# Kernel optimization log

Measured on AMD Instinct MI355X. Metric: run time of the kernel, lower is better.

Reference implementation:

```python
import jax, jax.numpy as jnp
import numpy as np

# Problem sizes (batched graph of G molecules)
N = 100_000   # total nodes
E = 400_000   # total directed edges
G = 2_500     # number of molecule graphs
K = 3         # len(idx_wo_smiles) -> zero rows inserted
NODE_F = 74   # graph_feats_shape[0]
EDGE_F = 12   # graph_feats_shape[1]
HID = 128     # hidden_feats = dim // 2
DIM = 256     # dim


def setup_inputs() -> dict:
    key = jax.random.key(0)
    ks = jax.random.split(key, 20)
    init = lambda k, shape, fan: (jax.random.normal(k, shape, jnp.float32) / np.sqrt(fan)).astype(jnp.float32)

    node_feats = jax.random.normal(ks[0], (N, NODE_F), jnp.float32)
    edge_feats = jax.random.normal(ks[1], (E, EDGE_F), jnp.float32)  # passed but unused by GCN
    src = jax.random.randint(ks[2], (E,), 0, N)
    dst = jax.random.randint(ks[3], (E,), 0, N)
    # sorted graph ids, every graph non-empty (~40 atoms each)
    graph_ids = (jnp.arange(N) * G) // N
    idx_wo_smiles = jnp.arange(K)

    return {
        'node_feats': node_feats,
        'edge_feats': edge_feats,
        'W1': init(ks[4], (NODE_F, HID), NODE_F), 'b1': jnp.zeros((HID,), jnp.float32),
        'Wr1': init(ks[5], (NODE_F, HID), NODE_F), 'br1': jnp.zeros((HID,), jnp.float32),
        'W2': init(ks[6], (HID, HID), HID), 'b2': jnp.zeros((HID,), jnp.float32),
        'Wr2': init(ks[7], (HID, HID), HID), 'br2': jnp.zeros((HID,), jnp.float32),
        'w_atom': init(ks[8], (HID, 1), HID), 'b_atom': jnp.zeros((1,), jnp.float32),
        'Wp1': init(ks[9], (2 * HID, HID), 2 * HID), 'bp1': jnp.zeros((HID,), jnp.float32),
        'Wp2': init(ks[10], (HID, DIM), HID), 'bp2': jnp.zeros((DIM,), jnp.float32),
        'src': src, 'dst': dst, 'graph_ids': graph_ids, 'idx_wo_smiles': idx_wo_smiles,
    }


def reference(node_feats, edge_feats, W1, b1, Wr1, br1, W2, b2, Wr2, br2,
              w_atom, b_atom, Wp1, bp1, Wp2, bp2, src, dst, graph_ids, idx_wo_smiles):
    n = node_feats.shape[0]
    ones_e = jnp.ones(src.shape[0], jnp.float32)
    out_deg = jax.ops.segment_sum(ones_e, src, num_segments=n)
    in_deg = jax.ops.segment_sum(ones_e, dst, num_segments=n)
    norm_s = jax.lax.rsqrt(jnp.maximum(out_deg, 1.0))  # [N]
    norm_d = jax.lax.rsqrt(jnp.maximum(in_deg, 1.0))   # [N]

    def gcn_layer(h, W, b, Wr, br):
        # GraphConv(norm='both'): D^-1/2 A D^-1/2 h W + b, with relu activation
        m = h[src] * norm_s[src][:, None]                       # [E, F] gather
        agg = jax.ops.segment_sum(m, dst, num_segments=n)       # [N, F] scatter-add
        gc = jax.nn.relu((agg * norm_d[:, None]) @ W + b)
        res = jax.nn.relu(h @ Wr + br)                          # residual connection
        return gc + res

    h = gcn_layer(node_feats, W1, b1, Wr1, br1)   # [N, HID]
    h = gcn_layer(h, W2, b2, Wr2, br2)            # [N, HID]

    # WeightedSumAndMax readout per molecule
    aw = jax.nn.sigmoid(h @ w_atom + b_atom)                          # [N, 1]
    hsum = jax.ops.segment_sum(h * aw, graph_ids, num_segments=G)     # [G, HID]
    hmax = jax.ops.segment_max(h, graph_ids, num_segments=G)          # [G, HID]
    gfeat = jnp.concatenate([hsum, hmax], axis=1)                     # [G, 2*HID]

    latent = jax.nn.relu(gfeat @ Wp1 + bp1) @ Wp2 + bp2               # [G, DIM]

    # Insert zero rows at idx_wo_smiles (sorted ascending -> final positions)
    total = G + idx_wo_smiles.shape[0]
    zero_mask = jnp.zeros((total,), bool).at[idx_wo_smiles].set(True)
    keep = jnp.nonzero(~zero_mask, size=G)[0]
    out = jnp.zeros((total, latent.shape[1]), latent.dtype).at[keep].set(latent)
    return out
```

## Files before the change

### kernel.cpp

```cpp
#include <hip/hip_runtime.h>
#include <hip/hip_bf16.h>
#include <stdint.h>

#define NODE_F 74
#define HID 128
#define DIM 256

typedef __hip_bfloat16 bf16;
typedef unsigned int u32;
typedef unsigned short u16;

typedef short s16x8 __attribute__((ext_vector_type(8)));
typedef __bf16 bf16x8 __attribute__((ext_vector_type(8)));
typedef float f32x4 __attribute__((ext_vector_type(4)));

__device__ __forceinline__ float rdl(float v, int l){
  return __int_as_float(__builtin_amdgcn_readlane(__float_as_int(v), l));
}
__device__ __forceinline__ float2 bfpair(u32 u){
  float2 r;
  r.x = __uint_as_float(u << 16);
  r.y = __uint_as_float(u & 0xffff0000u);
  return r;
}
__device__ __forceinline__ u32 packbf(float a, float b){
  u32 lo = (u32)__bfloat16_as_ushort(__float2bfloat16(a));
  u32 hi = (u32)__bfloat16_as_ushort(__float2bfloat16(b));
  return lo | (hi << 16);
}
__device__ __forceinline__ u16 bfbits(float a){
  return __bfloat16_as_ushort(__float2bfloat16(a));
}

__global__ void k_deg_prep(const int* __restrict__ src, const int* __restrict__ dst_,
                           float* __restrict__ outdeg_f, int* __restrict__ indeg, int E_,
                           const float* __restrict__ W1, const float* __restrict__ Wr1,
                           const float* __restrict__ W2, const float* __restrict__ Wr2,
                           u16* __restrict__ Bp1, u16* __restrict__ Bp2){
  int e = blockIdx.x*256 + threadIdx.x;
  if (e < E_){
    atomicAdd(&outdeg_f[src[e]], 1.0f);
    atomicAdd(&indeg[dst_[e]], 1);
  }
  int idx = e;
  if (idx < 57344){
    const float* W; u16* dstp; int S, Ktrue, loc;
    if      (idx < 12288){ W = W1;  dstp = Bp1;          S = 3; Ktrue = NODE_F; loc = idx; }
    else if (idx < 24576){ W = Wr1; dstp = Bp1 + 12288;  S = 3; Ktrue = NODE_F; loc = idx - 12288; }
    else if (idx < 40960){ W = W2;  dstp = Bp2;          S = 4; Ktrue = HID;    loc = idx - 24576; }
    else                 { W = Wr2; dstp = Bp2 + 16384;  S = 4; Ktrue = HID;    loc = idx - 40960; }
    const int el  = loc & 7;
    const int l   = (loc >> 3) & 63;
    const int rem = loc >> 9;
    const int s   = rem % S;
    const int t   = rem / S;
    const int k   = s*32 + (l >> 4)*8 + el;
    const int c   = t*16 + (l & 15);
    const float v = (k < Ktrue) ? W[(size_t)k*HID + c] : 0.f;
    dstp[loc] = bfbits(v);
  }
}

__global__ __launch_bounds__(256) void k_scan_a(const int* __restrict__ indeg,
                                                float* __restrict__ norm_s,
                                                float* __restrict__ norm_d,
                                                int* __restrict__ bsum, int n){
  __shared__ int red[256];
  const int base = blockIdx.x*1024 + threadIdx.x*4;
  int s = 0;
  #pragma unroll
  for (int i = 0; i < 4; ++i){
    const int idx = base + i;
    if (idx < n){
      const int d = indeg[idx];
      s += d;
      norm_d[idx] = rsqrtf(fmaxf((float)d, 1.0f));
      norm_s[idx] = rsqrtf(fmaxf(norm_s[idx], 1.0f));
    }
  }
  red[threadIdx.x] = s;
  __syncthreads();
  #pragma unroll
  for (int off = 128; off; off >>= 1){
    if (threadIdx.x < off) red[threadIdx.x] += red[threadIdx.x + off];
    __syncthreads();
  }
  if (threadIdx.x == 0) bsum[blockIdx.x] = red[0];
}

__global__ __launch_bounds__(1024) void k_scan_b(int* __restrict__ bsum, int nb){
  __shared__ int part[1024];
  __shared__ int carry;
  if (threadIdx.x == 0) carry = 0;
  __syncthreads();
  for (int c0 = 0; c0 < nb; c0 += 1024){
    const int tid = threadIdx.x, idx = c0 + tid;
    part[tid] = (idx < nb) ? bsum[idx] : 0;
    __syncthreads();
    for (int off = 1; off < 1024; off <<= 1){
      const int t = (tid >= off) ? part[tid-off] : 0;
      __syncthreads();
      part[tid] += t;
      __syncthreads();
    }
    if (idx < nb) bsum[idx] = carry + ((tid == 0) ? 0 : part[tid-1]);
    __syncthreads();
    if (tid == 0) carry += part[1023];
    __syncthreads();
  }
}

__global__ __launch_bounds__(256) void k_scan_c(int* __restrict__ indeg,
                                                const int* __restrict__ bsum,
                                                int* __restrict__ row_ptr, int n){
  __shared__ int part[256];
  const int base = blockIdx.x*1024 + threadIdx.x*4;
  int v[4]; int s = 0;
  #pragma unroll
  for (int i = 0; i < 4; ++i){
    const int idx = base + i;
    v[i] = (idx < n) ? indeg[idx] : 0;
    s += v[i];
  }
  part[threadIdx.x] = s;
  __syncthreads();
  for (int off = 1; off < 256; off <<= 1){
    const int t = (threadIdx.x >= off) ? part[threadIdx.x-off] : 0;
    __syncthreads();
    part[threadIdx.x] += t;
    __syncthreads();
  }
  int run = bsum[blockIdx.x] + ((threadIdx.x == 0) ? 0 : part[threadIdx.x-1]);
  #pragma unroll
  for (int i = 0; i < 4; ++i){
    const int idx = base + i;
    if (idx < n){
      row_ptr[idx] = run;
      run += v[i];
      indeg[idx] = 0;
    }
    if (idx == n-1) row_ptr[n] = run;
  }
}

__global__ void k_fill_conv(const int* __restrict__ src, const int* __restrict__ dst,
                            const int* __restrict__ row_ptr, int* __restrict__ cursor,
                            int* __restrict__ col, int E_,
                            const float* __restrict__ x0,
                            const float* __restrict__ norm_s,
                            u32* __restrict__ x0bf, int n, int do_conv){
  int e = blockIdx.x*256 + threadIdx.x;
  if (e < E_){
    int d = dst[e];
    int pos = row_ptr[d] + atomicAdd(&cursor[d], 1);
    col[pos] = src[e];
  }
  if (do_conv){
    const int tot = n*48;
    if (e < tot){
      const int r = e/48, l = e - r*48;
      const int f0 = 2*l, f1 = 2*l + 1;
      const float ns = norm_s[r];
      const float u0 = (f0 < NODE_F) ? ns*x0[(size_t)r*NODE_F + f0] : 0.f;
      const float u1 = (f1 < NODE_F) ? ns*x0[(size_t)r*NODE_F + f1] : 0.f;
      x0bf[e] = packbf(u0, u1);
    }
  }
}

__global__ __launch_bounds__(256, 8) void k_gather1b(
    const u32* __restrict__ x0bf, const int* __restrict__ row_ptr,
    const int* __restrict__ col, const float* __restrict__ norm_d,
    u32* __restrict__ ag1, int n){
  const int lane = threadIdx.x & 63;
  const int wv   = (blockIdx.x*256 + threadIdx.x) >> 6;
  const int r0   = wv*2;
  if (r0 >= n) return;
  int p[2], e[2];
  p[0] = row_ptr[r0]; e[0] = row_ptr[r0+1];
  const bool ok1 = (r0+1) < n;
  p[1] = ok1 ? e[0] : 0;
  e[1] = ok1 ? row_ptr[r0+2] : 0;
  const bool act = (lane < 48);
  const u32* xb = x0bf + lane;
  float a0[2] = {0.f,0.f}, a1[2] = {0.f,0.f};
  while ((p[0] < e[0]) | (p[1] < e[1])){
    int c[2], s[2][4];
    #pragma unroll
    for (int i = 0; i < 2; ++i){
      int d = e[i] - p[i];
      c[i] = (d > 4) ? 4 : ((d < 0) ? 0 : d);
      if (c[i] > 0){
        #pragma unroll
        for (int j = 0; j < 4; ++j)
          s[i][j] = col[p[i] + ((j < c[i]) ? j : (c[i]-1))];
      }
    }
    u32 v[2][4];
    #pragma unroll
    for (int i = 0; i < 2; ++i){
      #pragma unroll
      for (int j = 0; j < 4; ++j) v[i][j] = 0u;
      if (c[i] > 0 && act){
        #pragma unroll
        for (int j = 0; j < 4; ++j){
          const u32 t = xb[(size_t)s[i][j]*48];
          v[i][j] = (j < c[i]) ? t : 0u;
        }
      }
    }
    #pragma unroll
    for (int i = 0; i < 2; ++i){
      const float2 f0 = bfpair(v[i][0]), f1 = bfpair(v[i][1]);
      const float2 f2 = bfpair(v[i][2]), f3 = bfpair(v[i][3]);
      a0[i] += (f0.x + f1.x) + (f2.x + f3.x);
      a1[i] += (f0.y + f1.y) + (f2.y + f3.y);
      p[i] += c[i];
    }
  }
  if (lane < 48){
    #pragma unroll
    for (int i = 0; i < 2; ++i){
      const int row = r0 + i;
      if (row < n){
        const float nd = norm_d[row];
        ag1[(size_t)row*48 + lane] = packbf(a0[i]*nd, a1[i]*nd);
      }
    }
  }
}

__global__ __launch_bounds__(256, 8) void k_gather2b(
    const u32* __restrict__ h1u, const int* __restrict__ row_ptr,
    const int* __restrict__ col, const float* __restrict__ norm_s,
    const float* __restrict__ norm_d, u32* __restrict__ ag2, int n){
  const int lane = threadIdx.x & 63;
  const int wv   = (blockIdx.x*256 + threadIdx.x) >> 6;
  const int r0   = wv*2;
  if (r0 >= n) return;
  int p[2], e[2];
  p[0] = row_ptr[r0]; e[0] = row_ptr[r0+1];
  const bool ok1 = (r0+1) < n;
  p[1] = ok1 ? e[0] : 0;
  e[1] = ok1 ? row_ptr[r0+2] : 0;
  const u32* hb = h1u + lane;
  float a0[2] = {0.f,0.f}, a1[2] = {0.f,0.f};
  while ((p[0] < e[0]) | (p[1] < e[1])){
    int c[2], s[2][4];
    #pragma unroll
    for (int i = 0; i < 2; ++i){
      int d = e[i] - p[i];
      c[i] = (d > 4) ? 4 : ((d < 0) ? 0 : d);
      if (c[i] > 0){
        #pragma unroll
        for (int j = 0; j < 4; ++j)
          s[i][j] = col[p[i] + ((j < c[i]) ? j : (c[i]-1))];
      }
    }
    float nw[2][4];
    u32 v[2][4];
    #pragma unroll
    for (int i = 0; i < 2; ++i){
      #pragma unroll
      for (int j = 0; j < 4; ++j){ nw[i][j] = 0.f; v[i][j] = 0u; }
      if (c[i] > 0){
        #pragma unroll
        for (int j = 0; j < 4; ++j) nw[i][j] = (j < c[i]) ? norm_s[s[i][j]] : 0.f;
        #pragma unroll
        for (int j = 0; j < 4; ++j) v[i][j] = hb[(size_t)s[i][j]*64];
      }
    }
    #pragma unroll
    for (int i = 0; i < 2; ++i){
      const float2 f0 = bfpair(v[i][0]), f1 = bfpair(v[i][1]);
      const float2 f2 = bfpair(v[i][2]), f3 = bfpair(v[i][3]);
      a0[i] = fmaf(f0.x, nw[i][0], fmaf(f1.x, nw[i][1],
              fmaf(f2.x, nw[i][2], fmaf(f3.x, nw[i][3], a0[i]))));
      a1[i] = fmaf(f0.y, nw[i][0], fmaf(f1.y, nw[i][1],
              fmaf(f2.y, nw[i][2], fmaf(f3.y, nw[i][3], a1[i]))));
      p[i] += c[i];
    }
  }
  #pragma unroll
  for (int i = 0; i < 2; ++i){
    const int row = r0 + i;
    if (row < n){
      const float nd = norm_d[row];
      ag2[(size_t)row*64 + lane] = packbf(a0[i]*nd, a1[i]*nd);
    }
  }
}

__global__ __launch_bounds__(256) void k_gather1f(
    const float* __restrict__ x0, const int* __restrict__ row_ptr,
    const int* __restrict__ col, const float* __restrict__ norm_s,
    const float* __restrict__ norm_d, u32* __restrict__ ag1, int n){
  const int lane = threadIdx.x & 63;
  const int row  = blockIdx.x*4 + (threadIdx.x >> 6);
  if (row >= n) return;
  const int p0 = row_ptr[row], p1 = row_ptr[row+1];
  const bool act = (lane < 37);
  const float* xb = x0 + 2*lane;
  float a0 = 0.f, a1 = 0.f;
  int p = p0;
  #pragma unroll 1
  for (; p + 3 < p1; p += 4){
    const int s0 = col[p], s1 = col[p+1], s2 = col[p+2], s3 = col[p+3];
    const float n0 = norm_s[s0], n1 = norm_s[s1], n2 = norm_s[s2], n3 = norm_s[s3];
    float2 v0{0.f,0.f}, v1{0.f,0.f}, v2{0.f,0.f}, v3{0.f,0.f};
    if (act){
      v0 = *(const float2*)&xb[(size_t)s0*NODE_F];
      v1 = *(const float2*)&xb[(size_t)s1*NODE_F];
      v2 = *(const float2*)&xb[(size_t)s2*NODE_F];
      v3 = *(const float2*)&xb[(size_t)s3*NODE_F];
    }
    a0 = fmaf(v0.x,n0, fmaf(v1.x,n1, fmaf(v2.x,n2, fmaf(v3.x,n3, a0))));
    a1 = fmaf(v0.y,n0, fmaf(v1.y,n1, fmaf(v2.y,n2, fmaf(v3.y,n3, a1))));
  }
  const int rem = p1 - p;
  if (rem > 0){
    const int s0 = col[p];
    int s1 = s0, s2 = s0;
    float n1 = 0.f, n2 = 0.f;
    const float n0 = norm_s[s0];
    if (rem > 1){ s1 = col[p+1]; n1 = norm_s[s1]; }
    if (rem > 2){ s2 = col[p+2]; n2 = norm_s[s2]; }
    float2 v0{0.f,0.f}, v1{0.f,0.f}, v2{0.f,0.f};
    if (act){
      v0 = *(const float2*)&xb[(size_t)s0*NODE_F];
      v1 = *(const float2*)&xb[(size_t)s1*NODE_F];
      v2 = *(const float2*)&xb[(size_t)s2*NODE_F];
    }
    a0 = fmaf(v0.x,n0, fmaf(v1.x,n1, fmaf(v2.x,n2, a0)));
    a1 = fmaf(v0.y,n0, fmaf(v1.y,n1, fmaf(v2.y,n2, a1)));
  }
  if (lane < 48){
    const float nd = norm_d[row];
    ag1[(size_t)row*48 + lane] = packbf(a0*nd, a1*nd);
  }
}

__global__ __launch_bounds__(256) void k_gather2f(
    const u32* __restrict__ h1u, const int* __restrict__ row_ptr,
    const int* __restrict__ col, const float* __restrict__ norm_s,
    const float* __restrict__ norm_d, u32* __restrict__ ag2, int n){
  const int lane = threadIdx.x & 63;
  const int row  = blockIdx.x*4 + (threadIdx.x >> 6);
  if (row >= n) return;
  const int p0 = row_ptr[row], p1 = row_ptr[row+1];
  const u32* hb = h1u + lane;
  float a0 = 0.f, a1 = 0.f;
  int p = p0;
  #pragma unroll 1
  for (; p + 3 < p1; p += 4){
    const int s0 = col[p], s1 = col[p+1], s2 = col[p+2], s3 = col[p+3];
    const float n0 = norm_s[s0], n1 = norm_s[s1], n2 = norm_s[s2], n3 = norm_s[s3];
    const u32 u0 = hb[(size_t)s0*64];
    const u32 u1 = hb[(size_t)s1*64];
    const u32 u2 = hb[(size_t)s2*64];
    const u32 u3 = hb[(size_t)s3*64];
    const float2 f0 = bfpair(u0), f1 = bfpair(u1), f2 = bfpair(u2), f3 = bfpair(u3);
    a0 = fmaf(f0.x,n0, fmaf(f1.x,n1, fmaf(f2.x,n2, fmaf(f3.x,n3, a0))));
    a1 = fmaf(f0.y,n0, fmaf(f1.y,n1, fmaf(f2.y,n2, fmaf(f3.y,n3, a1))));
  }
  const int rem = p1 - p;
  if (rem > 0){
    const int s0 = col[p];
    int s1 = s0, s2 = s0;
    float n1 = 0.f, n2 = 0.f;
    const float n0 = norm_s[s0];
    if (rem > 1){ s1 = col[p+1]; n1 = norm_s[s1]; }
    if (rem > 2){ s2 = col[p+2]; n2 = norm_s[s2]; }
    const u32 u0 = hb[(size_t)s0*64];
    const u32 u1 = hb[(size_t)s1*64];
    const u32 u2 = hb[(size_t)s2*64];
    const float2 f0 = bfpair(u0), f1 = bfpair(u1), f2 = bfpair(u2);
    a0 = fmaf(f0.x,n0, fmaf(f1.x,n1, fmaf(f2.x,n2, a0)));
    a1 = fmaf(f0.y,n0, fmaf(f1.y,n1, fmaf(f2.y,n2, a1)));
  }
  const float nd = norm_d[row];
  ag2[(size_t)row*64 + lane] = packbf(a0*nd, a1*nd);
}

__global__ __launch_bounds__(256) void k_ggemm1(
    const u16* __restrict__ ag1, const float* __restrict__ x0,
    const u16* __restrict__ Bp, const float* __restrict__ bg_,
    const float* __restrict__ br_, u16* __restrict__ h1, int n){
  const int lane = threadIdx.x & 63;
  const int wid  = threadIdx.x >> 6;
  const int jg = lane & 15, kg = lane >> 4;
  const int r0 = blockIdx.x*64 + wid*16;
  const int row = r0 + jg;
  const bool rok = row < n;
  const int kb = kg*8;
  const int rA = rok ? row : (n-1);

  bf16x8 ag[3], ar[3];
  #pragma unroll
  for (int s = 0; s < 3; ++s)
    ag[s] = __builtin_bit_cast(bf16x8, *(const s16x8*)&ag1[(size_t)rA*96 + s*32 + kb]);
  {
    const float* px = x0 + (size_t)rA*NODE_F;
    #pragma unroll
    for (int s = 0; s < 2; ++s)
      #pragma unroll
      for (int e = 0; e < 8; e += 2){
        const float2 w = *(const float2*)&px[s*32 + kb + e];
        ar[s][e]   = (__bf16)w.x;
        ar[s][e+1] = (__bf16)w.y;
      }
    #pragma unroll
    for (int e = 0; e < 8; ++e) ar[2][e] = (__bf16)0.f;
    if (kg == 0){
      #pragma unroll
      for (int e = 0; e < 8; e += 2){
        const float2 w = *(const float2*)&px[64 + e];
        ar[2][e]   = (__bf16)w.x;
        ar[2][e+1] = (__bf16)w.y;
      }
    } else if (kg == 1){
      const float2 w = *(const float2*)&px[72];
      ar[2][0] = (__bf16)w.x;
      ar[2][1] = (__bf16)w.y;
    }
  }

  f32x4 accg[8], accr[8];
  #pragma unroll
  for (int t = 0; t < 8; ++t){
    accg[t] = f32x4{0.f,0.f,0.f,0.f};
    accr[t] = f32x4{0.f,0.f,0.f,0.f};
  }
  constexpr int FR1 = 8*3*512;
  #pragma unroll
  for (int s = 0; s < 3; ++s){
    #pragma unroll
    for (int t = 0; t < 8; ++t){
      const bf16x8 bg = __builtin_bit_cast(bf16x8,
          *(const s16x8*)&Bp[((t*3 + s)*64 + lane)*8]);
      const bf16x8 br = __builtin_bit_cast(bf16x8,
          *(const s16x8*)&Bp[FR1 + ((t*3 + s)*64 + lane)*8]);
      accg[t] = __builtin_amdgcn_mfma_f32_16x16x32_bf16(ag[s], bg, accg[t], 0,0,0);
      accr[t] = __builtin_amdgcn_mfma_f32_16x16x32_bf16(ar[s], br, accr[t], 0,0,0);
    }
  }

  const int rowb = r0 + 4*kg;
  #pragma unroll
  for (int t = 0; t < 8; ++t){
    const int colc = t*16 + jg;
    const float bgv = bg_[colc], brv = br_[colc];
    #pragma unroll
    for (int r = 0; r < 4; ++r){
      const int row2 = rowb + r;
      if (row2 < n){
        const float o = fmaxf(accg[t][r] + bgv, 0.f) + fmaxf(accr[t][r] + brv, 0.f);
        h1[(size_t)row2*HID + colc] = bfbits(o);
      }
    }
  }
}

__global__ __launch_bounds__(256) void k_ggemm2(
    const u16* __restrict__ ag2, const u16* __restrict__ h1,
    const u16* __restrict__ Bp, const float* __restrict__ bg_,
    const float* __restrict__ br_,
    const float* __restrict__ w_atom, const float* __restrict__ b_atom,
    const int* __restrict__ gid,
    float* __restrict__ hsum, u32* __restrict__ hmax, int n){
  const int lane = threadIdx.x & 63;
  const int wid  = threadIdx.x >> 6;
  const int jg = lane & 15, kg = lane >> 4;
  const int r0 = blockIdx.x*64 + wid*16;
  const int row = r0 + jg;
  const bool rok = row < n;
  const int kb = kg*8;
  const int rA = rok ? row : (n-1);

  f32x4 accg[8], accr[8];
  #pragma unroll
  for (int t = 0; t < 8; ++t){
    accg[t] = f32x4{0.f,0.f,0.f,0.f};
    accr[t] = f32x4{0.f,0.f,0.f,0.f};
  }
  constexpr int FR2 = 8*4*512;
  #pragma unroll
  for (int s = 0; s < 4; ++s){
    const bf16x8 agf = __builtin_bit_cast(bf16x8,
        *(const s16x8*)&ag2[(size_t)rA*HID + s*32 + kb]);
    const bf16x8 arf = __builtin_bit_cast(bf16x8,
        *(const s16x8*)&h1[(size_t)rA*HID + s*32 + kb]);
    #pragma unroll
    for (int t = 0; t < 8; ++t){
      const bf16x8 bg = __builtin_bit_cast(bf16x8,
          *(const s16x8*)&Bp[((t*4 + s)*64 + lane)*8]);
      const bf16x8 br = __builtin_bit_cast(bf16x8,
          *(const s16x8*)&Bp[FR2 + ((t*4 + s)*64 + lane)*8]);
      accg[t] = __builtin_amdgcn_mfma_f32_16x16x32_bf16(agf, bg, accg[t], 0,0,0);
      accr[t] = __builtin_amdgcn_mfma_f32_16x16x32_bf16(arf, br, accr[t], 0,0,0);
    }
  }

  float o[8][4];
  #pragma unroll
  for (int t = 0; t < 8; ++t){
    const int colc = t*16 + jg;
    const float bgv = bg_[colc], brv = br_[colc];
    #pragma unroll
    for (int r = 0; r < 4; ++r)
      o[t][r] = fmaxf(accg[t][r] + bgv, 0.f) + fmaxf(accr[t][r] + brv, 0.f);
  }
  if (r0 < n){
    float wa[8];
    #pragma unroll
    for (int t = 0; t < 8; ++t) wa[t] = w_atom[t*16 + jg];
    const float ba = b_atom[0];
    const int rowb = r0 + 4*kg;
    float awv[4]; int gidr[4];
    #pragma unroll
    for (int r = 0; r < 4; ++r){
      const int row2 = rowb + r;
      float dot = 0.f;
      #pragma unroll
      for (int t = 0; t < 8; ++t) dot = fmaf(o[t][r], wa[t], dot);
      dot += __shfl_xor(dot, 1);
      dot += __shfl_xor(dot, 2);
      dot += __shfl_xor(dot, 4);
      dot += __shfl_xor(dot, 8);
      awv[r]  = 1.0f/(1.0f + __expf(-(dot + ba)));
      gidr[r] = (row2 < n) ? gid[row2] : -1;
    }
    const int rhi    = (r0 + 15 < n) ? (r0 + 15) : (n - 1);
    const int gfirst = gid[r0];
    const int glast  = gid[rhi];
    for (int g = gfirst; g <= glast; ++g){
      #pragma unroll
      for (int t = 0; t < 8; ++t){
        float sv = 0.f, mv = 0.f;
        #pragma unroll
        for (int r = 0; r < 4; ++r){
          const bool in = (gidr[r] == g);
          sv += in ? o[t][r]*awv[r] : 0.f;
          mv  = in ? fmaxf(mv, o[t][r]) : mv;
        }
        sv += __shfl_xor(sv, 16);
        sv += __shfl_xor(sv, 32);
        mv  = fmaxf(mv, __shfl_xor(mv, 16));
        mv  = fmaxf(mv, __shfl_xor(mv, 32));
        if (lane < 16){
          atomicAdd(&hsum[(size_t)g*HID + t*16 + jg], sv);
          atomicMax(&hmax[(size_t)g*HID + t*16 + jg], __float_as_uint(mv));
        }
      }
    }
  }
}

__global__ __launch_bounds__(256) void k_mlp(
    const float* __restrict__ hsum, const float* __restrict__ hmaxf,
    const float* __restrict__ Wp1, const float* __restrict__ bp1,
    const float* __restrict__ Wp2, const float* __restrict__ bp2,
    const int* __restrict__ idxw, int K_,
    float* __restrict__ out, int G_){
  const int lane = threadIdx.x & 63;
  const int row = blockIdx.x*4 + (threadIdx.x >> 6);
  if (blockIdx.x == 0){
    for (int j = 0; j < K_; ++j){
      const int zr = idxw[j];
      for (int i = threadIdx.x; i < DIM; i += 256)
        out[(size_t)zr*DIM + i] = 0.f;
    }
  }
  if (row >= G_) return;
  const int c = lane*2;
  float ra0 = hsum [(size_t)row*HID + lane];
  float ra1 = hsum [(size_t)row*HID + 64 + lane];
  float ra2 = hmaxf[(size_t)row*HID + lane];
  float ra3 = hmaxf[(size_t)row*HID + 64 + lane];
  float a0 = 0.f, a1 = 0.f;
  #pragma unroll 4
  for (int k = 0; k < 64; ++k){
    const float v0 = rdl(ra0,k), v1 = rdl(ra1,k), v2 = rdl(ra2,k), v3 = rdl(ra3,k);
    const float2 w0 = *(const float2*)&Wp1[(size_t)(k      )*HID + c];
    const float2 w1 = *(const float2*)&Wp1[(size_t)(k +  64)*HID + c];
    const float2 w2 = *(const float2*)&Wp1[(size_t)(k + 128)*HID + c];
    const float2 w3 = *(const float2*)&Wp1[(size_t)(k + 192)*HID + c];
    a0 = fmaf(v0,w0.x, fmaf(v1,w1.x, fmaf(v2,w2.x, fmaf(v3,w3.x, a0))));
    a1 = fmaf(v0,w0.y, fmaf(v1,w1.y, fmaf(v2,w2.y, fmaf(v3,w3.y, a1))));
  }
  const float h0  = fmaxf(a0 + bp1[c],   0.f);
  const float h1v = fmaxf(a1 + bp1[c+1], 0.f);
  const int c4 = lane*4;
  float acc0=0.f, acc1=0.f, acc2=0.f, acc3=0.f;
  #pragma unroll 4
  for (int j = 0; j < 64; ++j){
    const float he = rdl(h0, j);
    const float ho = rdl(h1v, j);
    const float4 we = *(const float4*)&Wp2[(size_t)(2*j  )*DIM + c4];
    const float4 wo = *(const float4*)&Wp2[(size_t)(2*j+1)*DIM + c4];
    acc0 = fmaf(he,we.x, fmaf(ho,wo.x, acc0));
    acc1 = fmaf(he,we.y, fmaf(ho,wo.y, acc1));
    acc2 = fmaf(he,we.z, fmaf(ho,wo.z, acc2));
    acc3 = fmaf(he,we.w, fmaf(ho,wo.w, acc3));
  }
  int orow = row;
  for (int j = 0; j < K_; ++j){ if (idxw[j] <= orow) orow++; }
  float* po = out + (size_t)orow*DIM + c4;
  po[0] = acc0 + bp2[c4];
  po[1] = acc1 + bp2[c4+1];
  po[2] = acc2 + bp2[c4+2];
  po[3] = acc3 + bp2[c4+3];
}

extern "C" void kernel_launch(void* const* d_in, const int* in_sizes, int n_in,
                              void* d_out, int out_size, void* d_ws, size_t ws_size,
                              hipStream_t stream){
  (void)n_in;
  const float* x0     = (const float*)d_in[0];
  const float* W1     = (const float*)d_in[2];
  const float* b1     = (const float*)d_in[3];
  const float* Wr1    = (const float*)d_in[4];
  const float* br1    = (const float*)d_in[5];
  const float* W2     = (const float*)d_in[6];
  const float* b2     = (const float*)d_in[7];
  const float* Wr2    = (const float*)d_in[8];
  const float* br2    = (const float*)d_in[9];
  const float* w_atom = (const float*)d_in[10];
  const float* b_atom = (const float*)d_in[11];
  const float* Wp1    = (const float*)d_in[12];
  const float* bp1    = (const float*)d_in[13];
  const float* Wp2    = (const float*)d_in[14];
  const float* bp2    = (const float*)d_in[15];
  const int* src  = (const int*)d_in[16];
  const int* dst  = (const int*)d_in[17];
  const int* gid  = (const int*)d_in[18];
  const int* idxw = (const int*)d_in[19];

  const int N_ = in_sizes[0] / NODE_F;
  const int E_ = in_sizes[16];
  const int K_ = in_sizes[19];
  const int G_ = out_size / DIM - K_;

  u16*   h1     = (u16*)d_ws;
  float* norm_d = (float*)(h1 + (size_t)N_*HID);
  float* norm_s = norm_d + N_;
  float* hsum   = norm_s + N_;
  float* hmaxv  = hsum + (size_t)G_*HID;
  int*   indeg  = (int*)(hmaxv + (size_t)G_*HID);
  int*   row_ptr= indeg + N_;
  int*   col    = row_ptr + ((N_ + 4) & ~3);
  int*   bsum   = col + ((E_ + 4) & ~3);
  const int nscan = (N_ + 1023)/1024;
  uintptr_t aggp = ((uintptr_t)(bsum + nscan) + 255) & ~(uintptr_t)255;
  u32* aggu = (u32*)aggp;
  uintptr_t x0bfp = aggp + (size_t)N_*64*sizeof(u32);
  u32* x0bf = (u32*)x0bfp;
  const size_t need_bf = (x0bfp + (size_t)N_*48*sizeof(u32)) - (uintptr_t)d_ws;
  const bool use_bf = (ws_size >= need_bf);

  u16*   Bp1    = (u16*)d_out;
  u16*   Bp2    = Bp1 + 2*12288;

  hipMemsetAsync(norm_s, 0, ((size_t)2*N_ + (size_t)2*G_*HID)*sizeof(float), stream);

  k_deg_prep<<<(E_+255)/256, 256, 0, stream>>>(src, dst, norm_s, indeg, E_,
                                               W1, Wr1, W2, Wr2, Bp1, Bp2);
  k_scan_a  <<<nscan, 256, 0, stream>>>(indeg, norm_s, norm_d, bsum, N_);
  k_scan_b  <<<1, 1024, 0, stream>>>(bsum, nscan);
  k_scan_c  <<<nscan, 256, 0, stream>>>(indeg, bsum, row_ptr, N_);

  const int conv_tot = use_bf ? (N_*48 > E_ ? N_*48 : E_) : E_;
  k_fill_conv<<<(conv_tot+255)/256, 256, 0, stream>>>(
      src, dst, row_ptr, indeg, col, E_, x0, norm_s,
      use_bf ? x0bf : aggu, N_, use_bf ? 1 : 0);

  const int nb   = (N_ + 63) / 64;
  const int nbw  = (N_ + 3) / 4;
  const int nbw2 = (N_ + 7) / 8;
  if (use_bf){
    k_gather1b<<<nbw2, 256, 0, stream>>>(x0bf, row_ptr, col, norm_d, aggu, N_);
  } else {
    k_gather1f<<<nbw, 256, 0, stream>>>(x0, row_ptr, col, norm_s, norm_d, aggu, N_);
  }
  k_ggemm1<<<nb, 256, 0, stream>>>((const u16*)aggu, x0, Bp1, b1, br1, h1, N_);
  if (use_bf){
    k_gather2b<<<nbw2, 256, 0, stream>>>((const u32*)h1, row_ptr, col, norm_s,
                                         norm_d, aggu, N_);
  } else {
    k_gather2f<<<nbw, 256, 0, stream>>>((const u32*)h1, row_ptr, col, norm_s,
                                        norm_d, aggu, N_);
  }
  k_ggemm2<<<nb, 256, 0, stream>>>((const u16*)aggu, h1, Bp2, b2, br2,
                                   w_atom, b_atom, gid, hsum, (u32*)hmaxv, N_);

  k_mlp<<<(G_+3)/4, 256, 0, stream>>>(hsum, hmaxv, Wp1, bp1, Wp2, bp2,
                                      idxw, K_, (float*)d_out, G_);
}
```

Baseline: 367.5 us.

## Stage GEMM weights in LDS and use persistent grid-stride blocks

Both GCN GEMM kernels now copy the packed bf16 weight fragments into shared memory once per block, and each block loops over several 64-row tiles with a capped grid (768 and 512 blocks). This is meant to cut repeated global and L2 loads of the weight matrix by every tile, and to spread the one-time LDS fill across many tiles. The cost is 48–64 KB of LDS per block, which limits how many blocks fit on a CU and so reduces latency hiding for the row gathers. The early-exit `continue` sits inside the loop in ggemm2, which relies on the pooling tail having no barriers.

```diff
diff --git a/kernel.cpp b/kernel.cpp
--- a/kernel.cpp
+++ b/kernel.cpp
@@ -386,76 +386,89 @@
     const u16* __restrict__ ag1, const float* __restrict__ x0,
     const u16* __restrict__ Bp, const float* __restrict__ bg_,
     const float* __restrict__ br_, u16* __restrict__ h1, int n){
+  constexpr int FR1 = 8*3*512;
+  __shared__ __align__(16) u16 sB[2*FR1];
+  {
+    const uint4* s4 = (const uint4*)Bp;
+    uint4* d4 = (uint4*)sB;
+    #pragma unroll
+    for (int i = 0; i < 12; ++i)
+      d4[threadIdx.x + i*256] = s4[threadIdx.x + i*256];
+  }
+  __syncthreads();
   const int lane = threadIdx.x & 63;
   const int wid  = threadIdx.x >> 6;
   const int jg = lane & 15, kg = lane >> 4;
-  const int r0 = blockIdx.x*64 + wid*16;
-  const int row = r0 + jg;
-  const bool rok = row < n;
   const int kb = kg*8;
-  const int rA = rok ? row : (n-1);
-
-  bf16x8 ag[3], ar[3];
-  #pragma unroll
-  for (int s = 0; s < 3; ++s)
-    ag[s] = __builtin_bit_cast(bf16x8, *(const s16x8*)&ag1[(size_t)rA*96 + s*32 + kb]);
-  {
-    const float* px = x0 + (size_t)rA*NODE_F;
-    #pragma unroll
-    for (int s = 0; s < 2; ++s)
-      #pragma unroll
-      for (int e = 0; e < 8; e += 2){
-        const float2 w = *(const float2*)&px[s*32 + kb + e];
-        ar[s][e]   = (__bf16)w.x;
-        ar[s][e+1] = (__bf16)w.y;
-      }
-    #pragma unroll
-    for (int e = 0; e < 8; ++e) ar[2][e] = (__bf16)0.f;
-    if (kg == 0){
-      #pragma unroll
-      for (int e = 0; e < 8; e += 2){
-        const float2 w = *(const float2*)&px[64 + e];
-        ar[2][e]   = (__bf16)w.x;
-        ar[2][e+1] = (__bf16)w.y;
-      }
-    } else if (kg == 1){
-      const float2 w = *(const float2*)&px[72];
-      ar[2][0] = (__bf16)w.x;
-      ar[2][1] = (__bf16)w.y;
-    }
-  }
-
-  f32x4 accg[8], accr[8];
-  #pragma unroll
-  for (int t = 0; t < 8; ++t){
-    accg[t] = f32x4{0.f,0.f,0.f,0.f};
-    accr[t] = f32x4{0.f,0.f,0.f,0.f};
-  }
-  constexpr int FR1 = 8*3*512;
-  #pragma unroll
-  for (int s = 0; s < 3; ++s){
+  const int nb = (n + 63) >> 6;
+  for (int bt = blockIdx.x; bt < nb; bt += gridDim.x){
+    const int r0 = bt*64 + wid*16;
+    if (r0 >= n) continue;
+    const int row = r0 + jg;
+    const bool rok = row < n;
+    const int rA = rok ? row : (n-1);
+
+    bf16x8 ag[3], ar[3];
+    #pragma unroll
+    for (int s = 0; s < 3; ++s)
+      ag[s] = __builtin_bit_cast(bf16x8, *(const s16x8*)&ag1[(size_t)rA*96 + s*32 + kb]);
+    {
+      const float* px = x0 + (size_t)rA*NODE_F;
+      #pragma unroll
+      for (int s = 0; s < 2; ++s)
+        #pragma unroll
+        for (int e = 0; e < 8; e += 2){
+          const float2 w = *(const float2*)&px[s*32 + kb + e];
+          ar[s][e]   = (__bf16)w.x;
+          ar[s][e+1] = (__bf16)w.y;
+        }
+      #pragma unroll
+      for (int e = 0; e < 8; ++e) ar[2][e] = (__bf16)0.f;
+      if (kg == 0){
+        #pragma unroll
+        for (int e = 0; e < 8; e += 2){
+          const float2 w = *(const float2*)&px[64 + e];
+          ar[2][e]   = (__bf16)w.x;
+          ar[2][e+1] = (__bf16)w.y;
+        }
+      } else if (kg == 1){
+        const float2 w = *(const float2*)&px[72];
+        ar[2][0] = (__bf16)w.x;
+        ar[2][1] = (__bf16)w.y;
+      }
+    }
+
+    f32x4 accg[8], accr[8];
     #pragma unroll
     for (int t = 0; t < 8; ++t){
-      const bf16x8 bg = __builtin_bit_cast(bf16x8,
-          *(const s16x8*)&Bp[((t*3 + s)*64 + lane)*8]);
-      const bf16x8 br = __builtin_bit_cast(bf16x8,
-          *(const s16x8*)&Bp[FR1 + ((t*3 + s)*64 + lane)*8]);
-      accg[t] = __builtin_amdgcn_mfma_f32_16x16x32_bf16(ag[s], bg, accg[t], 0,0,0);
-      accr[t] = __builtin_amdgcn_mfma_f32_16x16x32_bf16(ar[s], br, accr[t], 0,0,0);
-    }
-  }
-
-  const int rowb = r0 + 4*kg;
-  #pragma unroll
-  for (int t = 0; t < 8; ++t){
-    const int colc = t*16 + jg;
-    const float bgv = bg_[colc], brv = br_[colc];
-    #pragma unroll
-    for (int r = 0; r < 4; ++r){
-      const int row2 = rowb + r;
-      if (row2 < n){
-        const float o = fmaxf(accg[t][r] + bgv, 0.f) + fmaxf(accr[t][r] + brv, 0.f);
-        h1[(size_t)row2*HID + colc] = bfbits(o);
+      accg[t] = f32x4{0.f,0.f,0.f,0.f};
+      accr[t] = f32x4{0.f,0.f,0.f,0.f};
+    }
+    #pragma unroll
+    for (int s = 0; s < 3; ++s){
+      #pragma unroll
+      for (int t = 0; t < 8; ++t){
+        const bf16x8 bg = __builtin_bit_cast(bf16x8,
+            *(const s16x8*)&sB[((t*3 + s)*64 + lane)*8]);
+        const bf16x8 br = __builtin_bit_cast(bf16x8,
+            *(const s16x8*)&sB[FR1 + ((t*3 + s)*64 + lane)*8]);
+        accg[t] = __builtin_amdgcn_mfma_f32_16x16x32_bf16(ag[s], bg, accg[t], 0,0,0);
+        accr[t] = __builtin_amdgcn_mfma_f32_16x16x32_bf16(ar[s], br, accr[t], 0,0,0);
+      }
+    }
+
+    const int rowb = r0 + 4*kg;
+    #pragma unroll
+    for (int t = 0; t < 8; ++t){
+      const int colc = t*16 + jg;
+      const float bgv = bg_[colc], brv = br_[colc];
+      #pragma unroll
+      for (int r = 0; r < 4; ++r){
+        const int row2 = rowb + r;
+        if (row2 < n){
+          const float o = fmaxf(accg[t][r] + bgv, 0.f) + fmaxf(accr[t][r] + brv, 0.f);
+          h1[(size_t)row2*HID + colc] = bfbits(o);
+        }
       }
     }
   }
@@ -468,49 +481,60 @@
     const float* __restrict__ w_atom, const float* __restrict__ b_atom,
     const int* __restrict__ gid,
     float* __restrict__ hsum, u32* __restrict__ hmax, int n){
+  constexpr int FR2 = 8*4*512;
+  __shared__ __align__(16) u16 sB[2*FR2];
+  {
+    const uint4* s4 = (const uint4*)Bp;
+    uint4* d4 = (uint4*)sB;
+    #pragma unroll
+    for (int i = 0; i < 16; ++i)
+      d4[threadIdx.x + i*256] = s4[threadIdx.x + i*256];
+  }
+  __syncthreads();
   const int lane = threadIdx.x & 63;
   const int wid  = threadIdx.x >> 6;
   const int jg = lane & 15, kg = lane >> 4;
-  const int r0 = blockIdx.x*64 + wid*16;
-  const int row = r0 + jg;
-  const bool rok = row < n;
   const int kb = kg*8;
-  const int rA = rok ? row : (n-1);
-
-  f32x4 accg[8], accr[8];
-  #pragma unroll
-  for (int t = 0; t < 8; ++t){
-    accg[t] = f32x4{0.f,0.f,0.f,0.f};
-    accr[t] = f32x4{0.f,0.f,0.f,0.f};
-  }
-  constexpr int FR2 = 8*4*512;
-  #pragma unroll
-  for (int s = 0; s < 4; ++s){
-    const bf16x8 agf = __builtin_bit_cast(bf16x8,
-        *(const s16x8*)&ag2[(size_t)rA*HID + s*32 + kb]);
-    const bf16x8 arf = __builtin_bit_cast(bf16x8,
-        *(const s16x8*)&h1[(size_t)rA*HID + s*32 + kb]);
+  const int nb = (n + 63) >> 6;
+  for (int bt = blockIdx.x; bt < nb; bt += gridDim.x){
+    const int r0 = bt*64 + wid*16;
+    if (r0 >= n) continue;
+    const int row = r0 + jg;
+    const bool rok = row < n;
+    const int rA = rok ? row : (n-1);
+
+    f32x4 accg[8], accr[8];
     #pragma unroll
     for (int t = 0; t < 8; ++t){
-      const bf16x8 bg = __builtin_bit_cast(bf16x8,
-          *(const s16x8*)&Bp[((t*4 + s)*64 + lane)*8]);
-      const bf16x8 br = __builtin_bit_cast(bf16x8,
-          *(const s16x8*)&Bp[FR2 + ((t*4 + s)*64 + lane)*8]);
-      accg[t] = __builtin_amdgcn_mfma_f32_16x16x32_bf16(agf, bg, accg[t], 0,0,0);
-      accr[t] = __builtin_amdgcn_mfma_f32_16x16x32_bf16(arf, br, accr[t], 0,0,0);
-    }
-  }
-
-  float o[8][4];
-  #pragma unroll
-  for (int t = 0; t < 8; ++t){
-    const int colc = t*16 + jg;
-    const float bgv = bg_[colc], brv = br_[colc];
-    #pragma unroll
-    for (int r = 0; r < 4; ++r)
-      o[t][r] = fmaxf(accg[t][r] + bgv, 0.f) + fmaxf(accr[t][r] + brv, 0.f);
-  }
-  if (r0 < n){
+      accg[t] = f32x4{0.f,0.f,0.f,0.f};
+      accr[t] = f32x4{0.f,0.f,0.f,0.f};
+    }
+    #pragma unroll
+    for (int s = 0; s < 4; ++s){
+      const bf16x8 agf = __builtin_bit_cast(bf16x8,
+          *(const s16x8*)&ag2[(size_t)rA*HID + s*32 + kb]);
+      const bf16x8 arf = __builtin_bit_cast(bf16x8,
+          *(const s16x8*)&h1[(size_t)rA*HID + s*32 + kb]);
+      #pragma unroll
+      for (int t = 0; t < 8; ++t){
+        const bf16x8 bg = __builtin_bit_cast(bf16x8,
+            *(const s16x8*)&sB[((t*4 + s)*64 + lane)*8]);
+        const bf16x8 br = __builtin_bit_cast(bf16x8,
+            *(const s16x8*)&sB[FR2 + ((t*4 + s)*64 + lane)*8]);
+        accg[t] = __builtin_amdgcn_mfma_f32_16x16x32_bf16(agf, bg, accg[t], 0,0,0);
+        accr[t] = __builtin_amdgcn_mfma_f32_16x16x32_bf16(arf, br, accr[t], 0,0,0);
+      }
+    }
+
+    float o[8][4];
+    #pragma unroll
+    for (int t = 0; t < 8; ++t){
+      const int colc = t*16 + jg;
+      const float bgv = bg_[colc], brv = br_[colc];
+      #pragma unroll
+      for (int r = 0; r < 4; ++r)
+        o[t][r] = fmaxf(accg[t][r] + bgv, 0.f) + fmaxf(accr[t][r] + brv, 0.f);
+    }
     float wa[8];
     #pragma unroll
     for (int t = 0; t < 8; ++t) wa[t] = w_atom[t*16 + jg];
@@ -677,12 +701,14 @@
   const int nb   = (N_ + 63) / 64;
   const int nbw  = (N_ + 3) / 4;
   const int nbw2 = (N_ + 7) / 8;
+  const int g1   = (nb < 768) ? nb : 768;
+  const int g2   = (nb < 512) ? nb : 512;
   if (use_bf){
     k_gather1b<<<nbw2, 256, 0, stream>>>(x0bf, row_ptr, col, norm_d, aggu, N_);
   } else {
     k_gather1f<<<nbw, 256, 0, stream>>>(x0, row_ptr, col, norm_s, norm_d, aggu, N_);
   }
-  k_ggemm1<<<nb, 256, 0, stream>>>((const u16*)aggu, x0, Bp1, b1, br1, h1, N_);
+  k_ggemm1<<<g1, 256, 0, stream>>>((const u16*)aggu, x0, Bp1, b1, br1, h1, N_);
   if (use_bf){
     k_gather2b<<<nbw2, 256, 0, stream>>>((const u32*)h1, row_ptr, col, norm_s,
                                          norm_d, aggu, N_);
@@ -690,7 +716,7 @@
     k_gather2f<<<nbw, 256, 0, stream>>>((const u32*)h1, row_ptr, col, norm_s,
                                         norm_d, aggu, N_);
   }
-  k_ggemm2<<<nb, 256, 0, stream>>>((const u16*)aggu, h1, Bp2, b2, br2,
+  k_ggemm2<<<g2, 256, 0, stream>>>((const u16*)aggu, h1, Bp2, b2, br2,
                                    w_atom, b_atom, gid, hsum, (u32*)hmaxv, N_);
 
   k_mlp<<<(G_+3)/4, 256, 0, stream>>>(hsum, hmaxv, Wp1, bp1, Wp2, bp2,
```

After: 337.8 us. 8.1% less time.
